# Kernel optimization log

Hardware: AMD Instinct MI355X
Metric: run time of the kernel (lower is better)

## Reference

```python
import jax, jax.numpy as jnp
import numpy as np

N_E = 8192
E_DIM = 256
BETA = 0.25
ORTHO_COEF = 1.0


def setup_inputs() -> dict:
    key = jax.random.key(0)
    k1, k2 = jax.random.split(key)
    z = jax.random.normal(k1, (16, E_DIM, 32, 32), dtype=jnp.float32)
    # nn.Embedding init: uniform(-1/n_e, 1/n_e)
    codebook = jax.random.uniform(k2, (N_E, E_DIM), dtype=jnp.float32,
                                  minval=-1.0 / N_E, maxval=1.0 / N_E)
    return {"z": z, "codebook": codebook}


def reference(z, codebook):
    B, C, H, W = z.shape
    n_e = codebook.shape[0]
    zt = jnp.transpose(z, (0, 2, 3, 1))            # (B,H,W,C)
    zf = zt.reshape(-1, C)                          # (N,C)

    # L2 distances: ||z||^2 + ||e||^2 - 2 z.e
    d = (jnp.sum(zf * zf, axis=1, keepdims=True)
         + jnp.sum(codebook * codebook, axis=1)
         - 2.0 * jnp.matmul(zf, codebook.T))        # (N, n_e)
    idx = jnp.argmin(d, axis=1)                     # (N,)

    z_q_flat = codebook[idx]                        # gather == one-hot @ codebook
    z_q = z_q_flat.reshape(zt.shape)                # (B,H,W,C)

    sg = jax.lax.stop_gradient
    loss = (BETA * jnp.mean((sg(z_q) - zt) ** 2)
            + jnp.mean((z_q - sg(zt)) ** 2))

    # ortho regularizer (force_emb_len_1 == False branch)
    wn = codebook / jnp.linalg.norm(codebook, axis=1, keepdims=True)
    diff = jnp.matmul(wn, wn.T) - jnp.eye(n_e, dtype=codebook.dtype)
    ortho_reg_term = ORTHO_COEF * jnp.sum(diff ** 2) / (n_e ** 2)

    # straight-through estimator
    z_q_st = zt + sg(z_q - zt)

    # perplexity from mean one-hot usage
    N = zf.shape[0]
    counts = jnp.zeros((n_e,), dtype=zt.dtype).at[idx].add(1.0)
    e_mean = counts / N
    perplexity = jnp.exp(-jnp.sum(e_mean * jnp.log(e_mean + 1e-10)))

    z_q_out = jnp.transpose(z_q_st, (0, 3, 1, 2))   # (B,C,H,W)
    return z_q_out, loss, ortho_reg_term, perplexity, idx
```

## Files before the change

### kernel.cpp

```cpp
#include <hip/hip_runtime.h>
#include <hip/hip_bf16.h>
#include <math.h>


#define N_E     8192
#define C_DIM   256
#define N_VEC   16384
#define N_ELEM  4194304
#define MARGIN  6.0e-4f

#define WS_COUNTS   0
#define WS_M        32768
#define WS_ACCUM    294912
#define WS_LISTLEN  294928
#define WS_ZERO_BYTES 295184
#define WS_CE       295184
#define WS_RN       327952
#define WS_A        360720
#define WS_KEYS     426256
#define WS_LISTS    557328
#define WS_TILEMIN  4751632
#define WS_ZBF      8945936
#define WS_CBBF     17334544
#define WS_THR      21528848
#define WS_ZT       21594384

typedef short short8v __attribute__((ext_vector_type(8)));
typedef float f32x4  __attribute__((ext_vector_type(4)));

__device__ inline unsigned short f2bf(float f) {
    unsigned int x = __float_as_uint(f);
    return (unsigned short)((x + 0x7fffu + ((x >> 16) & 1u)) >> 16);
}

__device__ inline void gload16(const void* g, void* l) {
    __builtin_amdgcn_global_load_lds(
        (const __attribute__((address_space(1))) unsigned int*)g,
        (__attribute__((address_space(3))) unsigned int*)l, 16, 0, 0);
}

__global__ __launch_bounds__(256) void k_cbprep(const float* __restrict__ cb,
                                                float* __restrict__ ce,
                                                float* __restrict__ rn,
                                                unsigned short* __restrict__ cbbf) {
    int j = blockIdx.x;
    int tid = threadIdx.x;
    float v = cb[(size_t)j * C_DIM + tid];
    cbbf[(size_t)j * C_DIM + tid] = f2bf(v);
    float s = v * v;
    #pragma unroll
    for (int off = 32; off > 0; off >>= 1) s += __shfl_down(s, off, 64);
    __shared__ float sh[4];
    if ((tid & 63) == 0) sh[tid >> 6] = s;
    __syncthreads();
    if (tid == 0) {
        float t = sh[0] + sh[1] + sh[2] + sh[3];
        ce[j] = t;
        rn[j] = 1.0f / sqrtf(t);
    }
}

__global__ __launch_bounds__(256) void k_ztrans(const float* __restrict__ z,
                                                unsigned short* __restrict__ zbf,
                                                float* __restrict__ zT,
                                                float* __restrict__ A) {
    __shared__ float tile[64 * 260];
    const int tid = threadIdx.x;
    const int n0 = blockIdx.x * 64;
    const int b = n0 >> 10, hw0 = n0 & 1023;
    const float* zp = z + (size_t)b * 262144 + hw0;

    const int hw = tid & 63, cg = tid >> 6;
    #pragma unroll 8
    for (int p = 0; p < 64; ++p) {
        int c = p * 4 + cg;
        tile[hw * 260 + c] = zp[(size_t)c * 1024 + hw];
    }
    __syncthreads();

    if (tid < 64) {
        float a = 0.0f;
        #pragma unroll 8
        for (int c = 0; c < C_DIM; ++c) {
            float v = tile[tid * 260 + c];
            a = fmaf(v, v, a);
        }
        A[n0 + tid] = a;
    }

    const int r = tid >> 2, q = tid & 3;
    unsigned short* dst = zbf + (size_t)(n0 + r) * C_DIM + q * 64;
    float* dstT         = zT  + (size_t)(n0 + r) * C_DIM + q * 64;
    const float* src = &tile[r * 260 + q * 64];
    #pragma unroll
    for (int i = 0; i < 8; ++i) {
        f32x4 lo = *(const f32x4*)&src[i * 8];
        f32x4 hi = *(const f32x4*)&src[i * 8 + 4];
        *(f32x4*)&dstT[i * 8]     = lo;
        *(f32x4*)&dstT[i * 8 + 4] = hi;
        short8v u;
        #pragma unroll
        for (int x = 0; x < 4; ++x) { u[x] = (short)f2bf(lo[x]); u[4 + x] = (short)f2bf(hi[x]); }
        *(short8v*)(dst + i * 8) = u;
    }
}

__global__ __launch_bounds__(256) void k_mfma(const unsigned short* __restrict__ zbf,
                                              const unsigned short* __restrict__ cbbf,
                                              float* __restrict__ tilemin) {
    __shared__ unsigned short As[128 * 64];
    __shared__ unsigned short Bs[128 * 64];
    __shared__ float smin[128][2];

    const int tid = threadIdx.x;
    const int lin = blockIdx.x;
    const int x = lin & 7, r = lin >> 3;
    const int jp = r >> 7, q = r & 127;
    const int by = x * 16 + (q >> 3), bx = jp * 8 + (q & 7);
    const int n0 = by * 128, j0 = bx * 128;
    const int wave = tid >> 6, lane = tid & 63;
    const int wx = wave & 1, wy = wave >> 1;
    const int g = lane >> 4, c = lane & 15;

    const int lrow  = lane >> 3;
    const int lslot = (lane & 7) ^ lrow;
    const int rbase = wave * 32;

    f32x4 acc[4][4];
    #pragma unroll
    for (int i = 0; i < 4; ++i)
        #pragma unroll
        for (int j = 0; j < 4; ++j) acc[i][j] = (f32x4){0.f, 0.f, 0.f, 0.f};

    for (int kc = 0; kc < C_DIM; kc += 64) {
        __syncthreads();
        #pragma unroll
        for (int i = 0; i < 4; ++i) {
            const int row8 = rbase + i * 8;
            const unsigned short* ga =
                zbf  + (size_t)(n0 + row8 + lrow) * C_DIM + kc + lslot * 8;
            const unsigned short* gb =
                cbbf + (size_t)(j0 + row8 + lrow) * C_DIM + kc + lslot * 8;
            gload16(ga, &As[row8 * 64]);
            gload16(gb, &Bs[row8 * 64]);
        }
        __syncthreads();

        #pragma unroll
        for (int kk = 0; kk < 2; ++kk) {
            short8v a[4], b[4];
            #pragma unroll
            for (int f = 0; f < 4; ++f) {
                const int row = wy * 64 + f * 16 + c;
                a[f] = *(const short8v*)&As[row * 64 + (((kk * 4 + g) ^ (c & 7)) * 8)];
            }
            #pragma unroll
            for (int f = 0; f < 4; ++f) {
                const int row = wx * 64 + f * 16 + c;
                b[f] = *(const short8v*)&Bs[row * 64 + (((kk * 4 + g) ^ (c & 7)) * 8)];
            }
            #pragma unroll
            for (int nf = 0; nf < 4; ++nf)
                #pragma unroll
                for (int jf = 0; jf < 4; ++jf)
                    acc[nf][jf] = __builtin_amdgcn_mfma_f32_16x16x32_bf16(
                        a[nf], b[jf], acc[nf][jf], 0, 0, 0);
        }
    }

    #pragma unroll
    for (int nf = 0; nf < 4; ++nf) {
        #pragma unroll
        for (int rr = 0; rr < 4; ++rr) {
            float mx = acc[nf][0][rr];
            #pragma unroll
            for (int jf = 1; jf < 4; ++jf) mx = fmaxf(mx, acc[nf][jf][rr]);
            #pragma unroll
            for (int off = 1; off < 16; off <<= 1)
                mx = fmaxf(mx, __shfl_xor(mx, off, 64));
            if (c == 0) smin[wy * 64 + nf * 16 + g * 4 + rr][wx] = -2.0f * mx;
        }
    }
    __syncthreads();
    if (tid < 128)
        tilemin[(size_t)bx * N_VEC + n0 + tid] = fminf(smin[tid][0], smin[tid][1]);
}

__global__ __launch_bounds__(256) void k_rowmin(const float* __restrict__ tilemin,
                                               float* __restrict__ thr,
                                               unsigned long long* __restrict__ keys) {
    __shared__ float red[4][64];
    const int nl = threadIdx.x & 63, tg = threadIdx.x >> 6;
    const int n = blockIdx.x * 64 + nl;
    float m = 3.4e38f;
    #pragma unroll
    for (int i = 0; i < 16; ++i)
        m = fminf(m, tilemin[(size_t)(tg * 16 + i) * N_VEC + n]);
    red[tg][nl] = m;
    __syncthreads();
    if (tg == 0) {
        thr[n] = fminf(fminf(red[0][nl], red[1][nl]),
                       fminf(red[2][nl], red[3][nl])) + MARGIN;
        keys[n] = ~0ull;
    }
}

__global__ __launch_bounds__(256) void k_build(const float* __restrict__ tilemin,
                                               const float* __restrict__ thr,
                                               int* __restrict__ listlen,
                                               int* __restrict__ lists) {
    const int t = blockIdx.x;
    const int lane = threadIdx.x & 63;
    #pragma unroll
    for (int it = 0; it < 8; ++it) {
        int n = blockIdx.y * 2048 + it * 256 + threadIdx.x;
        bool qq = tilemin[(size_t)t * N_VEC + n] <= thr[n];
        unsigned long long mask = __ballot(qq);
        if (mask) {
            int ldr = __ffsll(mask) - 1;
            int base = 0;
            if (lane == ldr) base = atomicAdd(&listlen[t], __popcll(mask));
            base = __shfl(base, ldr, 64);
            if (qq) {
                int pre = __popcll(mask & ((1ull << lane) - 1ull));
                lists[t * N_VEC + base + pre] = n;
            }
        }
    }
}

__global__ __launch_bounds__(256) void k_refine2(const float* __restrict__ zT,
                                                 const float* __restrict__ cb,
                                                 const float* __restrict__ ce,
                                                 const float* __restrict__ A,
                                                 const int* __restrict__ listlen,
                                                 const int* __restrict__ lists,
                                                 unsigned long long* __restrict__ keys) {
    __shared__ float e_s[128 * 68];
    __shared__ float z_s[32 * 68];
    __shared__ int   rows_s[32];

    const int t = blockIdx.x;
    const int len = listlen[t];
    const int tid = threadIdx.x;
    const int jg = tid & 31, rg = tid >> 5;
    const int j0 = t * 128;

    for (int b0 = blockIdx.y * 32; b0 < len; b0 += 128 * 32) {
        const int nrows = min(32, len - b0);
        __syncthreads();
        if (tid < 32)
            rows_s[tid] = lists[t * N_VEC + b0 + min(tid, nrows - 1)];

        float acc[4][4];
        #pragma unroll
        for (int rr = 0; rr < 4; ++rr)
            #pragma unroll
            for (int jj = 0; jj < 4; ++jj) acc[rr][jj] = 0.0f;

        for (int kc = 0; kc < C_DIM; kc += 64) {
            __syncthreads();
            {
                int jr = tid >> 1, ko = (tid & 1) * 32;
                #pragma unroll
                for (int i = 0; i < 8; ++i)
                    *(float4*)&e_s[jr * 68 + ko + i * 4] =
                        *(const float4*)&cb[(size_t)(j0 + jr) * C_DIM + kc + ko + i * 4];
            }
            {
                int r = tid >> 3, ko = (tid & 7) * 8;
                const float* zp = &zT[(size_t)rows_s[r] * C_DIM + kc + ko];
                *(float4*)&z_s[r * 68 + ko]     = *(const float4*)&zp[0];
                *(float4*)&z_s[r * 68 + ko + 4] = *(const float4*)&zp[4];
            }
            __syncthreads();

            #pragma unroll
            for (int k4 = 0; k4 < 16; ++k4) {
                float4 ef[4], zf[4];
                #pragma unroll
                for (int jj = 0; jj < 4; ++jj)
                    ef[jj] = *(const float4*)&e_s[(jg + 32 * jj) * 68 + k4 * 4];
                #pragma unroll
                for (int rr = 0; rr < 4; ++rr)
                    zf[rr] = *(const float4*)&z_s[(rg * 4 + rr) * 68 + k4 * 4];
                #pragma unroll
                for (int kk = 0; kk < 4; ++kk)
                    #pragma unroll
                    for (int rr = 0; rr < 4; ++rr)
                        #pragma unroll
                        for (int jj = 0; jj < 4; ++jj)
                            acc[rr][jj] = fmaf(((const float*)&zf[rr])[kk],
                                               ((const float*)&ef[jj])[kk], acc[rr][jj]);
            }
        }

        #pragma unroll
        for (int rr = 0; rr < 4; ++rr) {
            const int n = rows_s[rg * 4 + rr];
            const float An = A[n];
            unsigned long long best = ~0ull;
            #pragma unroll
            for (int jj = 0; jj < 4; ++jj) {
                int j = j0 + jg + 32 * jj;
                float tt = An + ce[j];
                float d = fmaf(-2.0f, acc[rr][jj], tt);
                unsigned int sd = __float_as_uint(d);
                sd = (sd & 0x80000000u) ? ~sd : (sd | 0x80000000u);
                unsigned long long key = ((unsigned long long)sd << 32) | (unsigned)j;
                best = key < best ? key : best;
            }
            #pragma unroll
            for (int off = 16; off > 0; off >>= 1) {
                unsigned long long o = __shfl_xor(best, off, 64);
                best = o < best ? o : best;
            }
            if (jg == 0) atomicMin(&keys[n], best);
        }
    }
}

__global__ __launch_bounds__(256) void k_gather(const float* __restrict__ z,
                                                const float* __restrict__ cb,
                                                const unsigned long long* __restrict__ keys,
                                                float* __restrict__ out,
                                                float* __restrict__ out_idx,
                                                int* __restrict__ counts,
                                                double* __restrict__ sse) {
    int bh = blockIdx.x;
    int b = bh >> 5, h = bh & 31;
    int tid = threadIdx.x;
    __shared__ int sidx[32];
    if (tid < 32) {
        int n = b * 1024 + h * 32 + tid;
        unsigned long long k = keys[n];
        int idx = (int)(k & 0xFFFFFFFFull);
        sidx[tid] = idx;
        out_idx[n] = (float)idx;
        atomicAdd(&counts[idx], 1);
    }
    __syncthreads();
    int w = tid & 31, cy = tid >> 5;
    int jid = sidx[w];
    const float* cbr = cb + (size_t)jid * C_DIM;
    size_t zb = (size_t)b * 262144 + h * 32 + w;

    double acc = 0.0;
    #pragma unroll 4
    for (int cc = 0; cc < 32; ++cc) {
        int c = cc * 8 + cy;
        float e = cbr[c];
        size_t zi = zb + (size_t)c * 1024;
        float d = e - z[zi];
        out[zi] = e;
        acc += (double)(d * d);
    }
    #pragma unroll
    for (int off = 32; off > 0; off >>= 1) acc += __shfl_down(acc, off, 64);
    __shared__ double sh[4];
    if ((tid & 63) == 0) sh[tid >> 6] = acc;
    __syncthreads();
    if (tid == 0) atomicAdd(sse, sh[0] + sh[1] + sh[2] + sh[3]);
}

__global__ __launch_bounds__(256) void k_gram(const float* __restrict__ cb,
                                              const float* __restrict__ rn,
                                              float* __restrict__ M) {
    __shared__ float aT[64][68];
    __shared__ float bT[64][68];
    int k0 = blockIdx.x * 64, l0 = blockIdx.y * 64;
    int jc0 = blockIdx.z * 256;
    int tid = threadIdx.x;
    int tk = tid & 15, tl = tid >> 4;
    float acc[4][4];
    #pragma unroll
    for (int i = 0; i < 4; ++i)
        #pragma unroll
        for (int l = 0; l < 4; ++l) acc[i][l] = 0.0f;

    for (int jc = jc0; jc < jc0 + 256; jc += 64) {
        __syncthreads();
        {
            int kk = tid & 63, jj0 = tid >> 6;
            #pragma unroll
            for (int p = 0; p < 16; ++p) {
                int jj = p * 4 + jj0;
                float r = rn[jc + jj];
                const float* row = cb + (size_t)(jc + jj) * C_DIM;
                aT[jj][kk] = row[k0 + kk] * r;
                bT[jj][kk] = row[l0 + kk] * r;
            }
        }
        __syncthreads();
        #pragma unroll 8
        for (int jj = 0; jj < 64; ++jj) {
            float4 av = *(const float4*)&aT[jj][tk * 4];
            float4 bv = *(const float4*)&bT[jj][tl * 4];
            float a4[4] = {av.x, av.y, av.z, av.w};
            float b4[4] = {bv.x, bv.y, bv.z, bv.w};
            #pragma unroll
            for (int i = 0; i < 4; ++i)
                #pragma unroll
                for (int l = 0; l < 4; ++l)
                    acc[i][l] = fmaf(a4[i], b4[l], acc[i][l]);
        }
    }
    #pragma unroll
    for (int i = 0; i < 4; ++i)
        #pragma unroll
        for (int l = 0; l < 4; ++l)
            atomicAdd(&M[(size_t)(k0 + tk * 4 + i) * C_DIM + l0 + tl * 4 + l], acc[i][l]);
}

__global__ __launch_bounds__(256) void k_final(const float* __restrict__ M,
                                               const int* __restrict__ counts,
                                               const double* __restrict__ accum,
                                               float* __restrict__ out_scalars) {
    int tid = threadIdx.x;
    __shared__ double sh[4];

    double s = 0.0;
    for (int i = tid; i < C_DIM * C_DIM; i += 256) {
        double m = M[i];
        s += m * m;
    }
    #pragma unroll
    for (int off = 32; off > 0; off >>= 1) s += __shfl_down(s, off, 64);
    if ((tid & 63) == 0) sh[tid >> 6] = s;
    __syncthreads();
    double S = sh[0] + sh[1] + sh[2] + sh[3];
    __syncthreads();

    double H = 0.0;
    for (int j = tid; j < N_E; j += 256) {
        double p = counts[j] * (1.0 / (double)N_VEC);
        H += p * log(p + 1e-10);
    }
    #pragma unroll
    for (int off = 32; off > 0; off >>= 1) H += __shfl_down(H, off, 64);
    if ((tid & 63) == 0) sh[tid >> 6] = H;
    __syncthreads();

    if (tid == 0) {
        double Hs = sh[0] + sh[1] + sh[2] + sh[3];
        out_scalars[0] = (float)(1.25 * accum[0] / (double)N_ELEM);
        out_scalars[1] = (float)((S - (double)N_E) / ((double)N_E * N_E));
        out_scalars[2] = (float)exp(-Hs);
    }
}

extern "C" void kernel_launch(void* const* d_in, const int* in_sizes, int n_in,
                              void* d_out, int out_size, void* d_ws, size_t ws_size,
                              hipStream_t stream) {
    (void)in_sizes; (void)n_in; (void)out_size; (void)ws_size;
    const float* z  = (const float*)d_in[0];
    const float* cb = (const float*)d_in[1];
    float* out = (float*)d_out;

    char* ws = (char*)d_ws;
    int* counts            = (int*)(ws + WS_COUNTS);
    float* M               = (float*)(ws + WS_M);
    double* accum          = (double*)(ws + WS_ACCUM);
    int* listlen           = (int*)(ws + WS_LISTLEN);
    float* ce              = (float*)(ws + WS_CE);
    float* rn              = (float*)(ws + WS_RN);
    float* A               = (float*)(ws + WS_A);
    unsigned long long* keys = (unsigned long long*)(ws + WS_KEYS);
    int* lists             = (int*)(ws + WS_LISTS);
    float* tilemin         = (float*)(ws + WS_TILEMIN);
    unsigned short* zbf    = (unsigned short*)(ws + WS_ZBF);
    unsigned short* cbbf   = (unsigned short*)(ws + WS_CBBF);
    float* thr             = (float*)(ws + WS_THR);
    float* zT              = (float*)(ws + WS_ZT);

    float* out_scalars = out + N_ELEM;
    float* out_idx     = out + N_ELEM + 3;

    hipMemsetAsync(ws, 0, WS_ZERO_BYTES, stream);

    k_cbprep<<<N_E, 256, 0, stream>>>(cb, ce, rn, cbbf);
    k_ztrans<<<N_VEC / 64, 256, 0, stream>>>(z, zbf, zT, A);
    k_mfma<<<8192, 256, 0, stream>>>(zbf, cbbf, tilemin);
    k_rowmin<<<N_VEC / 64, 256, 0, stream>>>(tilemin, thr, keys);
    k_build<<<dim3(64, 8), 256, 0, stream>>>(tilemin, thr, listlen, lists);
    k_refine2<<<dim3(64, 128), 256, 0, stream>>>(zT, cb, ce, A, listlen, lists, keys);
    k_gather<<<512, 256, 0, stream>>>(z, cb, keys, out, out_idx, counts, accum);
    k_gram<<<dim3(4, 4, 32), 256, 0, stream>>>(cb, rn, M);
    k_final<<<1, 256, 0, stream>>>(M, counts, accum, out_scalars);
}
```

Baseline: 424.3 us.

## Fold Gram kernel into MFMA grid and parallelize final scalar reductions

```diff
diff --git a/kernel.cpp b/kernel.cpp
--- a/kernel.cpp
+++ b/kernel.cpp
@@ -12,18 +12,18 @@
 #define WS_COUNTS   0
 #define WS_M        32768
 #define WS_ACCUM    294912
-#define WS_LISTLEN  294928
-#define WS_ZERO_BYTES 295184
-#define WS_CE       295184
-#define WS_RN       327952
-#define WS_A        360720
-#define WS_KEYS     426256
-#define WS_LISTS    557328
-#define WS_TILEMIN  4751632
-#define WS_ZBF      8945936
-#define WS_CBBF     17334544
-#define WS_THR      21528848
-#define WS_ZT       21594384
+#define WS_LISTLEN  294944
+#define WS_ZERO_BYTES 295200
+#define WS_CE       295200
+#define WS_RN       327968
+#define WS_A        360736
+#define WS_KEYS     426272
+#define WS_LISTS    557344
+#define WS_TILEMIN  4751648
+#define WS_ZBF      8945952
+#define WS_CBBF     17334560
+#define WS_THR      21528864
+#define WS_ZT       21594400
 
 typedef short short8v __attribute__((ext_vector_type(8)));
 typedef float f32x4  __attribute__((ext_vector_type(4)));
@@ -107,83 +107,136 @@
 
 __global__ __launch_bounds__(256) void k_mfma(const unsigned short* __restrict__ zbf,
                                               const unsigned short* __restrict__ cbbf,
-                                              float* __restrict__ tilemin) {
-    __shared__ unsigned short As[128 * 64];
-    __shared__ unsigned short Bs[128 * 64];
-    __shared__ float smin[128][2];
-
+                                              const float* __restrict__ cb,
+                                              const float* __restrict__ rn,
+                                              float* __restrict__ tilemin,
+                                              float* __restrict__ M) {
+    __shared__ unsigned long long ldsraw[4352];
     const int tid = threadIdx.x;
-    const int lin = blockIdx.x;
-    const int x = lin & 7, r = lin >> 3;
-    const int jp = r >> 7, q = r & 127;
-    const int by = x * 16 + (q >> 3), bx = jp * 8 + (q & 7);
-    const int n0 = by * 128, j0 = bx * 128;
-    const int wave = tid >> 6, lane = tid & 63;
-    const int wx = wave & 1, wy = wave >> 1;
-    const int g = lane >> 4, c = lane & 15;
-
-    const int lrow  = lane >> 3;
-    const int lslot = (lane & 7) ^ lrow;
-    const int rbase = wave * 32;
-
-    f32x4 acc[4][4];
-    #pragma unroll
-    for (int i = 0; i < 4; ++i)
-        #pragma unroll
-        for (int j = 0; j < 4; ++j) acc[i][j] = (f32x4){0.f, 0.f, 0.f, 0.f};
-
-    for (int kc = 0; kc < C_DIM; kc += 64) {
+
+    if (blockIdx.x < 8192) {
+        unsigned short* As = (unsigned short*)ldsraw;
+        unsigned short* Bs = As + 128 * 64;
+        float (*smin)[2]   = (float(*)[2])(Bs + 128 * 64);
+
+        const int lin = blockIdx.x;
+        const int x = lin & 7, r = lin >> 3;
+        const int jp = r >> 7, q = r & 127;
+        const int by = x * 16 + (q >> 3), bx = jp * 8 + (q & 7);
+        const int n0 = by * 128, j0 = bx * 128;
+        const int wave = tid >> 6, lane = tid & 63;
+        const int wx = wave & 1, wy = wave >> 1;
+        const int g = lane >> 4, c = lane & 15;
+
+        const int lrow  = lane >> 3;
+        const int lslot = (lane & 7) ^ lrow;
+        const int rbase = wave * 32;
+
+        f32x4 acc[4][4];
+        #pragma unroll
+        for (int i = 0; i < 4; ++i)
+            #pragma unroll
+            for (int j = 0; j < 4; ++j) acc[i][j] = (f32x4){0.f, 0.f, 0.f, 0.f};
+
+        for (int kc = 0; kc < C_DIM; kc += 64) {
+            __syncthreads();
+            #pragma unroll
+            for (int i = 0; i < 4; ++i) {
+                const int row8 = rbase + i * 8;
+                const unsigned short* ga =
+                    zbf  + (size_t)(n0 + row8 + lrow) * C_DIM + kc + lslot * 8;
+                const unsigned short* gb =
+                    cbbf + (size_t)(j0 + row8 + lrow) * C_DIM + kc + lslot * 8;
+                gload16(ga, &As[row8 * 64]);
+                gload16(gb, &Bs[row8 * 64]);
+            }
+            __syncthreads();
+
+            #pragma unroll
+            for (int kk = 0; kk < 2; ++kk) {
+                short8v a[4], b[4];
+                #pragma unroll
+                for (int f = 0; f < 4; ++f) {
+                    const int row = wy * 64 + f * 16 + c;
+                    a[f] = *(const short8v*)&As[row * 64 + (((kk * 4 + g) ^ (c & 7)) * 8)];
+                }
+                #pragma unroll
+                for (int f = 0; f < 4; ++f) {
+                    const int row = wx * 64 + f * 16 + c;
+                    b[f] = *(const short8v*)&Bs[row * 64 + (((kk * 4 + g) ^ (c & 7)) * 8)];
+                }
+                #pragma unroll
+                for (int nf = 0; nf < 4; ++nf)
+                    #pragma unroll
+                    for (int jf = 0; jf < 4; ++jf)
+                        acc[nf][jf] = __builtin_amdgcn_mfma_f32_16x16x32_bf16(
+                            a[nf], b[jf], acc[nf][jf], 0, 0, 0);
+            }
+        }
+
+        #pragma unroll
+        for (int nf = 0; nf < 4; ++nf) {
+            #pragma unroll
+            for (int rr = 0; rr < 4; ++rr) {
+                float mx = acc[nf][0][rr];
+                #pragma unroll
+                for (int jf = 1; jf < 4; ++jf) mx = fmaxf(mx, acc[nf][jf][rr]);
+                #pragma unroll
+                for (int off = 1; off < 16; off <<= 1)
+                    mx = fmaxf(mx, __shfl_xor(mx, off, 64));
+                if (c == 0) smin[wy * 64 + nf * 16 + g * 4 + rr][wx] = -2.0f * mx;
+            }
+        }
         __syncthreads();
-        #pragma unroll
-        for (int i = 0; i < 4; ++i) {
-            const int row8 = rbase + i * 8;
-            const unsigned short* ga =
-                zbf  + (size_t)(n0 + row8 + lrow) * C_DIM + kc + lslot * 8;
-            const unsigned short* gb =
-                cbbf + (size_t)(j0 + row8 + lrow) * C_DIM + kc + lslot * 8;
-            gload16(ga, &As[row8 * 64]);
-            gload16(gb, &Bs[row8 * 64]);
-        }
-        __syncthreads();
-
-        #pragma unroll
-        for (int kk = 0; kk < 2; ++kk) {
-            short8v a[4], b[4];
-            #pragma unroll
-            for (int f = 0; f < 4; ++f) {
-                const int row = wy * 64 + f * 16 + c;
-                a[f] = *(const short8v*)&As[row * 64 + (((kk * 4 + g) ^ (c & 7)) * 8)];
-            }
-            #pragma unroll
-            for (int f = 0; f < 4; ++f) {
-                const int row = wx * 64 + f * 16 + c;
-                b[f] = *(const short8v*)&Bs[row * 64 + (((kk * 4 + g) ^ (c & 7)) * 8)];
-            }
-            #pragma unroll
-            for (int nf = 0; nf < 4; ++nf)
-                #pragma unroll
-                for (int jf = 0; jf < 4; ++jf)
-                    acc[nf][jf] = __builtin_amdgcn_mfma_f32_16x16x32_bf16(
-                        a[nf], b[jf], acc[nf][jf], 0, 0, 0);
-        }
-    }
-
-    #pragma unroll
-    for (int nf = 0; nf < 4; ++nf) {
-        #pragma unroll
-        for (int rr = 0; rr < 4; ++rr) {
-            float mx = acc[nf][0][rr];
-            #pragma unroll
-            for (int jf = 1; jf < 4; ++jf) mx = fmaxf(mx, acc[nf][jf][rr]);
-            #pragma unroll
-            for (int off = 1; off < 16; off <<= 1)
-                mx = fmaxf(mx, __shfl_xor(mx, off, 64));
-            if (c == 0) smin[wy * 64 + nf * 16 + g * 4 + rr][wx] = -2.0f * mx;
-        }
-    }
-    __syncthreads();
-    if (tid < 128)
-        tilemin[(size_t)bx * N_VEC + n0 + tid] = fminf(smin[tid][0], smin[tid][1]);
+        if (tid < 128)
+            tilemin[(size_t)bx * N_VEC + n0 + tid] = fminf(smin[tid][0], smin[tid][1]);
+
+    } else {
+        float* aT = (float*)ldsraw;
+        float* bT = aT + 64 * 68;
+        const int gidx = blockIdx.x - 8192;
+        const int k0 = (gidx & 3) * 64, l0 = ((gidx >> 2) & 3) * 64;
+        const int jc0 = (gidx >> 4) * 256;
+        const int tk = tid & 15, tl = tid >> 4;
+        float acc[4][4];
+        #pragma unroll
+        for (int i = 0; i < 4; ++i)
+            #pragma unroll
+            for (int l = 0; l < 4; ++l) acc[i][l] = 0.0f;
+
+        for (int jc = jc0; jc < jc0 + 256; jc += 64) {
+            __syncthreads();
+            {
+                int kk = tid & 63, jj0 = tid >> 6;
+                #pragma unroll
+                for (int p = 0; p < 16; ++p) {
+                    int jj = p * 4 + jj0;
+                    float rr = rn[jc + jj];
+                    const float* row = cb + (size_t)(jc + jj) * C_DIM;
+                    aT[jj * 68 + kk] = row[k0 + kk] * rr;
+                    bT[jj * 68 + kk] = row[l0 + kk] * rr;
+                }
+            }
+            __syncthreads();
+            #pragma unroll 8
+            for (int jj = 0; jj < 64; ++jj) {
+                float4 av = *(const float4*)&aT[jj * 68 + tk * 4];
+                float4 bv = *(const float4*)&bT[jj * 68 + tl * 4];
+                float a4[4] = {av.x, av.y, av.z, av.w};
+                float b4[4] = {bv.x, bv.y, bv.z, bv.w};
+                #pragma unroll
+                for (int i = 0; i < 4; ++i)
+                    #pragma unroll
+                    for (int l = 0; l < 4; ++l)
+                        acc[i][l] = fmaf(a4[i], b4[l], acc[i][l]);
+            }
+        }
+        #pragma unroll
+        for (int i = 0; i < 4; ++i)
+            #pragma unroll
+            for (int l = 0; l < 4; ++l)
+                atomicAdd(&M[(size_t)(k0 + tk * 4 + i) * C_DIM + l0 + tl * 4 + l], acc[i][l]);
+    }
 }
 
 __global__ __launch_bounds__(256) void k_rowmin(const float* __restrict__ tilemin,
@@ -363,89 +416,36 @@
     if (tid == 0) atomicAdd(sse, sh[0] + sh[1] + sh[2] + sh[3]);
 }
 
-__global__ __launch_bounds__(256) void k_gram(const float* __restrict__ cb,
-                                              const float* __restrict__ rn,
-                                              float* __restrict__ M) {
-    __shared__ float aT[64][68];
-    __shared__ float bT[64][68];
-    int k0 = blockIdx.x * 64, l0 = blockIdx.y * 64;
-    int jc0 = blockIdx.z * 256;
-    int tid = threadIdx.x;
-    int tk = tid & 15, tl = tid >> 4;
-    float acc[4][4];
-    #pragma unroll
-    for (int i = 0; i < 4; ++i)
-        #pragma unroll
-        for (int l = 0; l < 4; ++l) acc[i][l] = 0.0f;
-
-    for (int jc = jc0; jc < jc0 + 256; jc += 64) {
-        __syncthreads();
-        {
-            int kk = tid & 63, jj0 = tid >> 6;
-            #pragma unroll
-            for (int p = 0; p < 16; ++p) {
-                int jj = p * 4 + jj0;
-                float r = rn[jc + jj];
-                const float* row = cb + (size_t)(jc + jj) * C_DIM;
-                aT[jj][kk] = row[k0 + kk] * r;
-                bT[jj][kk] = row[l0 + kk] * r;
-            }
-        }
-        __syncthreads();
-        #pragma unroll 8
-        for (int jj = 0; jj < 64; ++jj) {
-            float4 av = *(const float4*)&aT[jj][tk * 4];
-            float4 bv = *(const float4*)&bT[jj][tl * 4];
-            float a4[4] = {av.x, av.y, av.z, av.w};
-            float b4[4] = {bv.x, bv.y, bv.z, bv.w};
-            #pragma unroll
-            for (int i = 0; i < 4; ++i)
-                #pragma unroll
-                for (int l = 0; l < 4; ++l)
-                    acc[i][l] = fmaf(a4[i], b4[l], acc[i][l]);
-        }
-    }
-    #pragma unroll
-    for (int i = 0; i < 4; ++i)
-        #pragma unroll
-        for (int l = 0; l < 4; ++l)
-            atomicAdd(&M[(size_t)(k0 + tk * 4 + i) * C_DIM + l0 + tl * 4 + l], acc[i][l]);
-}
-
-__global__ __launch_bounds__(256) void k_final(const float* __restrict__ M,
-                                               const int* __restrict__ counts,
-                                               const double* __restrict__ accum,
-                                               float* __restrict__ out_scalars) {
-    int tid = threadIdx.x;
+__global__ __launch_bounds__(256) void k_msq(const float* __restrict__ M,
+                                             const int* __restrict__ counts,
+                                             double* __restrict__ accum) {
+    const int tid = threadIdx.x, bid = blockIdx.x;
     __shared__ double sh[4];
-
     double s = 0.0;
-    for (int i = tid; i < C_DIM * C_DIM; i += 256) {
-        double m = M[i];
-        s += m * m;
+    if (bid < 64) {
+        const float* p = &M[bid * 1024 + tid * 4];
+        float4 v = *(const float4*)p;
+        s = (double)v.x * v.x + (double)v.y * v.y
+          + (double)v.z * v.z + (double)v.w * v.w;
+    } else {
+        int j = (bid - 64) * 256 + tid;
+        double p = counts[j] * (1.0 / (double)N_VEC);
+        s = p * log(p + 1e-10);
     }
     #pragma unroll
     for (int off = 32; off > 0; off >>= 1) s += __shfl_down(s, off, 64);
     if ((tid & 63) == 0) sh[tid >> 6] = s;
     __syncthreads();
-    double S = sh[0] + sh[1] + sh[2] + sh[3];
-    __syncthreads();
-
-    double H = 0.0;
-    for (int j = tid; j < N_E; j += 256) {
-        double p = counts[j] * (1.0 / (double)N_VEC);
-        H += p * log(p + 1e-10);
-    }
-    #pragma unroll
-    for (int off = 32; off > 0; off >>= 1) H += __shfl_down(H, off, 64);
-    if ((tid & 63) == 0) sh[tid >> 6] = H;
-    __syncthreads();
-
-    if (tid == 0) {
-        double Hs = sh[0] + sh[1] + sh[2] + sh[3];
+    if (tid == 0)
+        atomicAdd(&accum[bid < 64 ? 1 : 2], sh[0] + sh[1] + sh[2] + sh[3]);
+}
+
+__global__ __launch_bounds__(64) void k_final(const double* __restrict__ accum,
+                                              float* __restrict__ out_scalars) {
+    if (threadIdx.x == 0) {
         out_scalars[0] = (float)(1.25 * accum[0] / (double)N_ELEM);
-        out_scalars[1] = (float)((S - (double)N_E) / ((double)N_E * N_E));
-        out_scalars[2] = (float)exp(-Hs);
+        out_scalars[1] = (float)((accum[1] - (double)N_E) / ((double)N_E * N_E));
+        out_scalars[2] = (float)exp(-accum[2]);
     }
 }
 
@@ -480,11 +480,11 @@
 
     k_cbprep<<<N_E, 256, 0, stream>>>(cb, ce, rn, cbbf);
     k_ztrans<<<N_VEC / 64, 256, 0, stream>>>(z, zbf, zT, A);
-    k_mfma<<<8192, 256, 0, stream>>>(zbf, cbbf, tilemin);
+    k_mfma<<<8704, 256, 0, stream>>>(zbf, cbbf, cb, rn, tilemin, M);
     k_rowmin<<<N_VEC / 64, 256, 0, stream>>>(tilemin, thr, keys);
     k_build<<<dim3(64, 8), 256, 0, stream>>>(tilemin, thr, listlen, lists);
     k_refine2<<<dim3(64, 128), 256, 0, stream>>>(zT, cb, ce, A, listlen, lists, keys);
     k_gather<<<512, 256, 0, stream>>>(z, cb, keys, out, out_idx, counts, accum);
-    k_gram<<<dim3(4, 4, 32), 256, 0, stream>>>(cb, rn, M);
-    k_final<<<1, 256, 0, stream>>>(M, counts, accum, out_scalars);
-}
+    k_msq<<<96, 256, 0, stream>>>(M, counts, accum);
+    k_final<<<1, 64, 0, stream>>>(accum, out_scalars);
+}
```

Result: faster. 359.2 us (-15.3%).
